# Kernel tuning notes

Hardware: AMD Instinct MI355X
Metric: run time of the kernel (lower is better)

The kernel has to match this reference:

```python
import jax, jax.numpy as jnp
import numpy as np

N = 1024       # sentence length (words incl. root at index 0)
WD = 300       # word embedding dim (GloVe-style)
PD = 25        # pos_emb_dim
H = 125        # hidden_dim_lstm
FC = 100       # hidden_dim_fc
PVOCAB = 50    # POS tagset size


def setup_inputs() -> dict:
    key = jax.random.key(0)
    ks = jax.random.split(key, 14)
    f = lambda k, s: jax.random.normal(k, s, dtype=jnp.float32) * 0.1
    d_in = WD + PD
    return {
        "word_vecs": jax.random.normal(ks[0], (N, WD), dtype=jnp.float32),
        "pos_idx": jax.random.randint(ks[1], (N,), 0, PVOCAB),
        "parents_ids": jax.random.randint(ks[2], (N,), 0, N),
        "pos_emb": f(ks[3], (PVOCAB, PD)),
        "Wih0": f(ks[4], (2, 4 * H, d_in)),
        "Whh0": f(ks[5], (2, 4 * H, H)),
        "b0": f(ks[6], (2, 4 * H)),
        "Wih1": f(ks[7], (2, 4 * H, 2 * H)),
        "Whh1": f(ks[8], (2, 4 * H, H)),
        "b1": f(ks[9], (2, 4 * H)),
        "fc1_W": f(ks[10], (FC, 4 * H)),
        "fc1_b": f(ks[11], (FC,)),
        "fc2_W": f(ks[12], (1, FC)),
        "fc2_b": f(ks[13], (1,)),
    }


def _lstm_dir(x, Wih, Whh, b, reverse):
    # torch LSTM cell, gate order (i, f, g, o); b = b_ih + b_hh
    Hd = Whh.shape[1]
    def step(carry, xt):
        h, c = carry
        g = xt @ Wih.T + h @ Whh.T + b
        i, fg, gg, o = jnp.split(g, 4)
        i = jax.nn.sigmoid(i)
        fg = jax.nn.sigmoid(fg)
        gg = jnp.tanh(gg)
        o = jax.nn.sigmoid(o)
        c = fg * c + i * gg
        h = o * jnp.tanh(c)
        return (h, c), h
    init = (jnp.zeros((Hd,), x.dtype), jnp.zeros((Hd,), x.dtype))
    _, hs = jax.lax.scan(step, init, x, reverse=reverse)
    return hs  # [n, H], already in original time order


def _bilstm_layer(x, Wih, Whh, b):
    hf = _lstm_dir(x, Wih[0], Whh[0], b[0], False)
    hb = _lstm_dir(x, Wih[1], Whh[1], b[1], True)
    return jnp.concatenate([hf, hb], axis=1)  # [n, 2H]


def reference(word_vecs, pos_idx, parents_ids, pos_emb, Wih0, Whh0, b0,
              Wih1, Whh1, b1, fc1_W, fc1_b, fc2_W, fc2_b):
    # encoder: concat word + pos embeddings, 2-layer BiLSTM
    x = jnp.concatenate([word_vecs, pos_emb[pos_idx]], axis=1)  # [n, WD+PD]
    h = _bilstm_layer(x, Wih0, Whh0, b0)
    h = _bilstm_layer(h, Wih1, Whh1, b1)  # [n, 2H]
    n = h.shape[0]
    twoH = h.shape[1]
    # fc1(cat(h_i, h_j)) = h_i @ W_head^T + h_j @ W_child^T + b  (vectorized over all pairs)
    A = h @ fc1_W[:, :twoH].T   # head contribution  [n, FC]
    B = h @ fc1_W[:, twoH:].T   # child contribution [n, FC]
    T = jnp.tanh(A[:, None, :] + B[None, :, :] + fc1_b)  # [n, n, FC]
    raw = T @ fc2_W[0] + fc2_b[0]                         # [n, n]
    ii = jnp.arange(n)
    # original loop skips diagonal and arcs into the root (j == 0); those stay 0
    mask = (ii[:, None] != ii[None, :]) & (ii[None, :] != 0)
    scores_mat = jnp.where(mask, raw, jnp.float32(0.0))
    logits = scores_mat.T  # row j = scores of heads for child j
    logp = jax.nn.log_softmax(logits, axis=1)
    loss = -jnp.mean(logp[jnp.arange(n), parents_ids])
    return loss, scores_mat
```

## Files before the change

kernel.cpp:

```cpp
#include <hip/hip_runtime.h>

typedef float v2f __attribute__((ext_vector_type(2)));
typedef _Float16 f16x8 __attribute__((ext_vector_type(8)));
typedef float f32x4 __attribute__((ext_vector_type(4)));

#define LOG2E 1.4426950408889634f
#define LN2   0.6931471805599453f

__device__ __forceinline__ float fexp2(float x) {
  float r; asm("v_exp_f32 %0, %1" : "=v"(r) : "v"(x)); return r;
}
__device__ __forceinline__ float frcp(float x) {
  float r; asm("v_rcp_f32 %0, %1" : "=v"(r) : "v"(x)); return r;
}
__device__ __forceinline__ float flog2(float x) {
  float r; asm("v_log_f32 %0, %1" : "=v"(r) : "v"(x)); return r;
}
__device__ __forceinline__ void lgkm_barrier() {
  __builtin_amdgcn_sched_barrier(0);
  asm volatile("s_waitcnt lgkmcnt(0)" ::: "memory");
  __builtin_amdgcn_s_barrier();
  __builtin_amdgcn_sched_barrier(0);
}

__global__ void k_embed(const float* __restrict__ wv, const int* __restrict__ pidx,
                        const float* __restrict__ pemb, float* __restrict__ X) {
  int t = blockIdx.x;
  int pi = pidx[t];
  for (int c = threadIdx.x; c < 336; c += 128) {
    float v;
    if (c < 300)      v = wv[t * 300 + c];
    else if (c < 325) v = pemb[pi * 25 + (c - 300)];
    else              v = 0.f;
    X[t * 336 + c] = v;
  }
}

__global__ void k_repack(const float* __restrict__ src, float* __restrict__ dst,
                         int sK, int dK) {
  int r = blockIdx.x;
  for (int c = threadIdx.x; c < dK; c += 128)
    dst[r * dK + c] = (c < sK) ? src[r * sK + c] : 0.f;
}

__global__ void k_wab(const float* __restrict__ fc1W, float* __restrict__ Wab) {
  int r = blockIdx.x;
  int sr = (r < 100) ? r : r - 100;
  int so = (r < 100) ? 0 : 250;
  for (int c = threadIdx.x; c < 256; c += 128)
    Wab[r * 256 + c] = (c < 250) ? fc1W[sr * 500 + so + c] : 0.f;
}

__global__ void k_misc(const float* __restrict__ fc1b, const float* __restrict__ fc2W,
                       float* __restrict__ biasAB, float* __restrict__ sumw) {
  __shared__ float red[128];
  int t = threadIdx.x;
  for (int c = t; c < 256; c += 128)
    biasAB[c] = (c < 100) ? fc1b[c] : 0.f;
  float s = (t < 100) ? fc2W[t] : 0.f;
  red[t] = s; __syncthreads();
  for (int off = 64; off; off >>= 1) {
    if (t < off) red[t] += red[t + off];
    __syncthreads();
  }
  if (t == 0) sumw[0] = red[0];
}

#define BM 64
#define BN 64
#define BKK 16
__global__ __launch_bounds__(256) void k_gemm(
    const float* __restrict__ A, const float* __restrict__ Bw,
    const float* __restrict__ bias, float* __restrict__ C,
    int M, int N, int K, int ldC, long sBz, long sCz, long sbz, int transOut) {
  const int z = blockIdx.z;
  const float* Bp = Bw + (size_t)z * sBz;
  const float* bp = bias + (size_t)z * sbz;
  float* Cp = C + (size_t)z * sCz;
  const int bm = blockIdx.y * BM, bn = blockIdx.x * BN;
  __shared__ __align__(16) float As[BKK][BM + 4];
  __shared__ __align__(16) float Bs[BKK][BN + 4];
  __shared__ float Ts[BN][BM + 1];
  const int tid = threadIdx.x;
  const int tx = tid & 15, ty = tid >> 4;
  const int lr = tid >> 2;
  const int lk = (tid & 3) * 4;
  float acc[4][4];
#pragma unroll
  for (int a = 0; a < 4; ++a)
#pragma unroll
    for (int b = 0; b < 4; ++b) acc[a][b] = 0.f;

  int brow = bn + lr; if (brow >= N) brow = N - 1;
  for (int k0 = 0; k0 < K; k0 += BKK) {
    float4 a4 = *(const float4*)(A + (size_t)(bm + lr) * K + k0 + lk);
    float4 b4 = *(const float4*)(Bp + (size_t)brow * K + k0 + lk);
    __syncthreads();
    As[lk + 0][lr] = a4.x; As[lk + 1][lr] = a4.y; As[lk + 2][lr] = a4.z; As[lk + 3][lr] = a4.w;
    Bs[lk + 0][lr] = b4.x; Bs[lk + 1][lr] = b4.y; Bs[lk + 2][lr] = b4.z; Bs[lk + 3][lr] = b4.w;
    __syncthreads();
#pragma unroll
    for (int kk = 0; kk < BKK; ++kk) {
      float4 av = *(const float4*)&As[kk][ty * 4];
      float4 bv = *(const float4*)&Bs[kk][tx * 4];
      float aa[4] = {av.x, av.y, av.z, av.w};
      float bb[4] = {bv.x, bv.y, bv.z, bv.w};
#pragma unroll
      for (int a = 0; a < 4; ++a)
#pragma unroll
        for (int b = 0; b < 4; ++b)
          acc[a][b] = __builtin_fmaf(aa[a], bb[b], acc[a][b]);
    }
  }
  if (!transOut) {
#pragma unroll
    for (int a = 0; a < 4; ++a) {
      int i = bm + ty * 4 + a;
#pragma unroll
      for (int b = 0; b < 4; ++b) {
        int j = bn + tx * 4 + b;
        if (j < N) Cp[(size_t)i * ldC + j] = acc[a][b] + bp[j];
      }
    }
  } else {
    __syncthreads();
#pragma unroll
    for (int a = 0; a < 4; ++a)
#pragma unroll
      for (int b = 0; b < 4; ++b) {
        int jn = bn + tx * 4 + b; if (jn >= N) jn = N - 1;
        Ts[tx * 4 + b][ty * 4 + a] = acc[a][b] + bp[jn];
      }
    __syncthreads();
    const int n2 = tid >> 2, mq = (tid & 3) * 16;
    const int n = bn + n2;
    if (n < N) {
#pragma unroll
      for (int r = 0; r < 4; ++r) {
        int m0 = mq + r * 4;
        float4 v;
        v.x = Ts[n2][m0 + 0]; v.y = Ts[n2][m0 + 1];
        v.z = Ts[n2][m0 + 2]; v.w = Ts[n2][m0 + 3];
        *(float4*)(Cp + (size_t)n * ldC + bm + m0) = v;
      }
    }
  }
}

__global__ __launch_bounds__(512) void k_rec(const float* __restrict__ Pt,
                                             const float* __restrict__ Whh,
                                             float* __restrict__ hout) {
  const int d = blockIdx.x;
  const bool fwd = (d == 0);
  const int t = threadIdx.x;
  const int w  = t >> 6;
  const int l  = t & 63;
  const int lg = l >> 4;
  const int lc = l & 15;
  const int q  = lc >> 2;

  int u_p = t >> 2; const bool activep = (u_p < 125); if (u_p > 124) u_p = 124;
  const int sub = t & 3;
  const float4* Pr = (const float4*)(Pt + (size_t)d * 500 * 1024 +
                                     (size_t)(sub * 125 + u_p) * 1024);

  const float* Wd = Whh + (size_t)d * 500 * 125;
  f16x8 a[4][4];
#pragma unroll
  for (int rt = 0; rt < 4; ++rt) {
    const int rho = (w << 6) + (rt << 4) + lc;
    const int u2 = rho >> 2, g2 = rho & 3;
    const bool uok = (u2 < 125);
    const float* wr2 = Wd + (size_t)(g2 * 125 + (uok ? u2 : 0)) * 125;
#pragma unroll
    for (int kt = 0; kt < 4; ++kt) {
      f16x8 v;
#pragma unroll
      for (int j = 0; j < 8; ++j) {
        const int k = kt * 32 + lg * 8 + j;
        v[j] = (_Float16)((uok && k < 125) ? wr2[k] : 0.f);
      }
      a[rt][kt] = v;
    }
  }

  __shared__ __align__(16) _Float16 hf[2][128];
  __shared__ __align__(16) float preb[2][512];
  __shared__ float hist[32][128];
  for (int i = t; i < 128; i += 512) ((int*)hf)[i] = 0;
  for (int i = t; i < 1024; i += 512) ((float*)preb)[i] = 0.f;

  float4 cura = Pr[fwd ? 0 : 254];
  float4 curb = Pr[fwd ? 1 : 255];
  float cst = 0.f;
  if (activep) preb[0][t] = fwd ? cura.x : curb.w;
  __syncthreads();

  for (int cb = 0; cb < 128; ++cb) {
    const int nc = (cb + 1 < 128) ? cb + 1 : cb;
    float4 nxta = Pr[fwd ? 2 * nc     : 254 - 2 * nc];
    float4 nxtb = Pr[fwd ? 2 * nc + 1 : 255 - 2 * nc];
#pragma unroll
    for (int e = 0; e < 8; ++e) {
      const int buf = e & 1;
      f16x8 hfr[4];
#pragma unroll
      for (int kt = 0; kt < 4; ++kt)
        hfr[kt] = *(const f16x8*)&hf[buf][kt * 32 + lg * 8];
      f32x4 acc[4];
#pragma unroll
      for (int rt = 0; rt < 4; ++rt)
        acc[rt] = *(const f32x4*)&preb[buf][(w << 6) + (rt << 4) + (lg << 2)];
#pragma unroll
      for (int kt = 0; kt < 4; ++kt)
#pragma unroll
        for (int rt = 0; rt < 4; ++rt)
          acc[rt] = __builtin_amdgcn_mfma_f32_16x16x32_f16(a[rt][kt], hfr[kt],
                                                           acc[rt], 0, 0, 0);
      f32x4 T = (q == 0) ? acc[0] : (q == 1) ? acc[1] : (q == 2) ? acc[2] : acc[3];
      float gi = frcp(1.f + fexp2(-LOG2E * T[0]));
      float gf = frcp(1.f + fexp2(-LOG2E * T[1]));
      float gg = __builtin_fmaf(2.f, frcp(1.f + fexp2(-2.f * LOG2E * T[2])), -1.f);
      float go = frcp(1.f + fexp2(-LOG2E * T[3]));
      cst = __builtin_fmaf(gf, cst, gi * gg);
      float th = __builtin_fmaf(2.f, frcp(1.f + fexp2(-2.f * LOG2E * cst)), -1.f);
      float hv = go * th;
      float pf, pb2;
      if (e < 7) {
        pf  = (e == 0) ? cura.y : (e == 1) ? cura.z : (e == 2) ? cura.w
            : (e == 3) ? curb.x : (e == 4) ? curb.y : (e == 5) ? curb.z : curb.w;
        pb2 = (e == 0) ? curb.z : (e == 1) ? curb.y : (e == 2) ? curb.x
            : (e == 3) ? cura.w : (e == 4) ? cura.z : (e == 5) ? cura.y : cura.x;
      } else { pf = nxta.x; pb2 = nxtb.w; }
      const float pre_next = fwd ? pf : pb2;
      const int u_own = (w << 4) + (q << 2) + lg;
      if (((lc & 3) == 0) && u_own < 125) {
        hf[buf ^ 1][u_own] = (_Float16)hv;
        hist[(cb & 3) * 8 + e][u_own] = hv;
      }
      if (activep) preb[buf ^ 1][t] = pre_next;
      lgkm_barrier();
    }
    if ((cb & 3) == 3) {
      const int S0 = (cb - 3) * 8;
#pragma unroll
      for (int k = 0; k < 8; ++k) {
        int idx = t + k * 512;
        int r = idx >> 7, u2 = idx & 127;
        if (u2 < 125) {
          int step = S0 + r;
          int time = fwd ? step : 1023 - step;
          hout[(size_t)time * 256 + d * 125 + u2] = hist[r][u2];
        }
      }
      lgkm_barrier();
    }
    cura = nxta; curb = nxtb;
  }
}

__global__ __launch_bounds__(256) void k_pair(const float* __restrict__ AB,
    const float* __restrict__ fc2W, const float* __restrict__ fc2b,
    const float* __restrict__ sumw, float* __restrict__ outS,
    float* __restrict__ scoresT) {
  __shared__ float As[32][100];
  __shared__ float Bs[32][101];
  __shared__ float w2s[100];
  const int tid = threadIdx.x;
  const int i0 = blockIdx.y * 32, j0 = blockIdx.x * 32;
  for (int idx = tid; idx < 3200; idx += 256) {
    int r = idx / 100, k = idx - r * 100;
    As[r][k] = AB[(size_t)(i0 + r) * 200 + k];
    Bs[r][k] = AB[(size_t)(j0 + r) * 200 + 100 + k];
  }
  if (tid < 100) w2s[tid] = 2.f * fc2W[tid];
  __syncthreads();
  const int tx = tid & 31, ty = tid >> 5;
  float acc[4] = {0.f, 0.f, 0.f, 0.f};
#pragma unroll 4
  for (int k = 0; k < 100; ++k) {
    float b = Bs[tx][k];
    float wk2 = w2s[k];
    float bs = b * (2.f * LOG2E);
#pragma unroll
    for (int q = 0; q < 4; ++q) {
      float a = As[ty + 8 * q][k];
      float r = frcp(1.f + fexp2(__builtin_fmaf(a, 2.f * LOG2E, bs)));
      acc[q] = __builtin_fmaf(wk2, r, acc[q]);
    }
  }
  float base = sumw[0] + fc2b[0];
  const int j = j0 + tx;
#pragma unroll
  for (int q = 0; q < 4; ++q) {
    int i = i0 + ty + 8 * q;
    float val = (i != j && j != 0) ? (base - acc[q]) : 0.f;
    outS[(size_t)i * 1024 + j] = val;
    scoresT[(size_t)j * 1024 + i] = val;
  }
}

__global__ __launch_bounds__(256) void k_soft(const float* __restrict__ scoresT,
    const int* __restrict__ parents, float* __restrict__ contrib) {
  const int j = blockIdx.x, tid = threadIdx.x;
  __shared__ float red[256];
  const float* row = scoresT + (size_t)j * 1024;
  float v0 = row[tid], v1 = row[tid + 256], v2 = row[tid + 512], v3 = row[tid + 768];
  float m = fmaxf(fmaxf(v0, v1), fmaxf(v2, v3));
  red[tid] = m; __syncthreads();
  for (int off = 128; off; off >>= 1) {
    if (tid < off) red[tid] = fmaxf(red[tid], red[tid + off]);
    __syncthreads();
  }
  m = red[0]; __syncthreads();
  float s = fexp2((v0 - m) * LOG2E) + fexp2((v1 - m) * LOG2E) +
            fexp2((v2 - m) * LOG2E) + fexp2((v3 - m) * LOG2E);
  red[tid] = s; __syncthreads();
  for (int off = 128; off; off >>= 1) {
    if (tid < off) red[tid] += red[tid + off];
    __syncthreads();
  }
  if (tid == 0) {
    float S = red[0];
    int p = parents[j];
    contrib[j] = row[p] - m - flog2(S) * LN2;
  }
}

__global__ __launch_bounds__(256) void k_loss(const float* __restrict__ contrib,
                                              float* __restrict__ out) {
  __shared__ float red[256];
  int tid = threadIdx.x;
  float s = contrib[tid] + contrib[tid + 256] + contrib[tid + 512] + contrib[tid + 768];
  red[tid] = s; __syncthreads();
  for (int off = 128; off; off >>= 1) {
    if (tid < off) red[tid] += red[tid + off];
    __syncthreads();
  }
  if (tid == 0) out[0] = -red[0] * (1.f / 1024.f);
}

extern "C" void kernel_launch(void* const* d_in, const int* in_sizes, int n_in,
                              void* d_out, int out_size, void* d_ws, size_t ws_size,
                              hipStream_t stream) {
  const float* wv   = (const float*)d_in[0];
  const int*   pidx = (const int*)d_in[1];
  const int*   par  = (const int*)d_in[2];
  const float* pemb = (const float*)d_in[3];
  const float* Wih0 = (const float*)d_in[4];
  const float* Whh0 = (const float*)d_in[5];
  const float* b0   = (const float*)d_in[6];
  const float* Wih1 = (const float*)d_in[7];
  const float* Whh1 = (const float*)d_in[8];
  const float* b1   = (const float*)d_in[9];
  const float* fc1W = (const float*)d_in[10];
  const float* fc1b = (const float*)d_in[11];
  const float* fc2W = (const float*)d_in[12];
  const float* fc2b = (const float*)d_in[13];
  float* ws = (float*)d_ws;
  float* X      = ws + 0;
  float* Wih0p  = ws + 344064;
  float* Pt0    = ws + 680064;
  float* h0     = ws + 1704064;
  float* Wih1p  = ws + 1966208;
  float* Pt1    = ws + 2222208;
  float* h1     = ws + 3246208;
  float* Wab    = ws + 3508352;
  float* biasAB = ws + 3559552;
  float* AB     = ws + 3559808;
  float* scT    = ws + 3764608;
  float* contrib= ws + 4813184;
  float* sumw   = ws + 4814208;
  float* out = (float*)d_out;

  hipMemsetAsync(h0, 0, 1024 * 256 * sizeof(float), stream);
  hipMemsetAsync(h1, 0, 1024 * 256 * sizeof(float), stream);

  k_embed <<<1024, 128, 0, stream>>>(wv, pidx, pemb, X);
  k_repack<<<1000, 128, 0, stream>>>(Wih0, Wih0p, 325, 336);
  k_repack<<<1000, 128, 0, stream>>>(Wih1, Wih1p, 250, 256);
  k_wab   <<<200, 128, 0, stream>>>(fc1W, Wab);
  k_misc  <<<1, 128, 0, stream>>>(fc1b, fc2W, biasAB, sumw);

  k_gemm<<<dim3(8, 16, 2), 256, 0, stream>>>(X, Wih0p, b0, Pt0, 1024, 500, 336, 1024,
                                             500L * 336, 500L * 1024, 500L, 1);
  k_rec <<<2, 512, 0, stream>>>(Pt0, Whh0, h0);
  k_gemm<<<dim3(8, 16, 2), 256, 0, stream>>>(h0, Wih1p, b1, Pt1, 1024, 500, 256, 1024,
                                             500L * 256, 500L * 1024, 500L, 1);
  k_rec <<<2, 512, 0, stream>>>(Pt1, Whh1, h1);
  k_gemm<<<dim3(4, 16, 1), 256, 0, stream>>>(h1, Wab, biasAB, AB, 1024, 200, 256, 200,
                                             0L, 0L, 0L, 0);
  k_pair<<<dim3(32, 32), 256, 0, stream>>>(AB, fc2W, fc2b, sumw, out + 1, scT);
  k_soft<<<1024, 256, 0, stream>>>(scT, par, contrib);
  k_loss<<<1, 256, 0, stream>>>(contrib, out);
}
```

Measured before the change: 1.212 ms.

## Pre-permute gate rows and run recurrence with 1024 threads reading preacts directly

The input-projection weights and biases are repacked into the row order the recurrent MFMA tiles use, so the GEMM writes time-major preactivations that each lane can load directly as f32x4 accumulators. This removes the shared-memory preactivation staging buffer and its per-step stores. The recurrent kernel doubles to 1024 threads with two row tiles per wave instead of four, shortening each wave's serial MFMA chain per step. In exchange every step needs a global load on the critical path and the per-step barrier now spans 16 waves instead of 8.

```diff
diff --git a/kernel.cpp b/kernel.cpp
--- a/kernel.cpp
+++ b/kernel.cpp
@@ -36,11 +36,18 @@
   }
 }
 
-__global__ void k_repack(const float* __restrict__ src, float* __restrict__ dst,
-                         int sK, int dK) {
-  int r = blockIdx.x;
+__global__ void k_wpack(const float* __restrict__ Wih, const float* __restrict__ b,
+                        float* __restrict__ Wp, float* __restrict__ bp,
+                        int sK, int dK) {
+  const int d = blockIdx.y, rho = blockIdx.x;
+  const int u = rho >> 2, g = rho & 3;
+  const bool ok = (u < 125);
+  const float* src = Wih + ((size_t)d * 500 + g * 125 + (ok ? u : 0)) * sK;
+  float* dst = Wp + ((size_t)d * 512 + rho) * dK;
   for (int c = threadIdx.x; c < dK; c += 128)
-    dst[r * dK + c] = (c < sK) ? src[r * sK + c] : 0.f;
+    dst[c] = (ok && c < sK) ? src[c] : 0.f;
+  if (threadIdx.x == 0)
+    bp[d * 512 + rho] = ok ? b[d * 500 + g * 125 + u] : 0.f;
 }
 
 __global__ void k_wab(const float* __restrict__ fc1W, float* __restrict__ Wab) {
@@ -147,9 +154,9 @@
   }
 }
 
-__global__ __launch_bounds__(512) void k_rec(const float* __restrict__ Pt,
-                                             const float* __restrict__ Whh,
-                                             float* __restrict__ hout) {
+__global__ __launch_bounds__(1024) void k_rec(const float* __restrict__ Ptt,
+                                              const float* __restrict__ Whh,
+                                              float* __restrict__ hout) {
   const int d = blockIdx.x;
   const bool fwd = (d == 0);
   const int t = threadIdx.x;
@@ -157,18 +164,13 @@
   const int l  = t & 63;
   const int lg = l >> 4;
   const int lc = l & 15;
-  const int q  = lc >> 2;
-
-  int u_p = t >> 2; const bool activep = (u_p < 125); if (u_p > 124) u_p = 124;
-  const int sub = t & 3;
-  const float4* Pr = (const float4*)(Pt + (size_t)d * 500 * 1024 +
-                                     (size_t)(sub * 125 + u_p) * 1024);
+  const int rtsel = lc & 1;
 
   const float* Wd = Whh + (size_t)d * 500 * 125;
-  f16x8 a[4][4];
-#pragma unroll
-  for (int rt = 0; rt < 4; ++rt) {
-    const int rho = (w << 6) + (rt << 4) + lc;
+  f16x8 a[2][4];
+#pragma unroll
+  for (int rt = 0; rt < 2; ++rt) {
+    const int rho = (w << 5) + (rt << 4) + lc;
     const int u2 = rho >> 2, g2 = rho & 3;
     const bool uok = (u2 < 125);
     const float* wr2 = Wd + (size_t)(g2 * 125 + (uok ? u2 : 0)) * 125;
@@ -185,39 +187,36 @@
   }
 
   __shared__ __align__(16) _Float16 hf[2][128];
-  __shared__ __align__(16) float preb[2][512];
   __shared__ float hist[32][128];
-  for (int i = t; i < 128; i += 512) ((int*)hf)[i] = 0;
-  for (int i = t; i < 1024; i += 512) ((float*)preb)[i] = 0.f;
-
-  float4 cura = Pr[fwd ? 0 : 254];
-  float4 curb = Pr[fwd ? 1 : 255];
+  if (t < 128) ((int*)hf)[t] = 0;
+
+  const int dstep = fwd ? 512 : -512;
+  const float* pg = Ptt + (size_t)d * 1024 * 512 +
+                    (size_t)(fwd ? 0 : 1023) * 512 + ((w << 5) + (lg << 2));
+  f32x4 pc0 = *(const f32x4*)(pg);
+  f32x4 pc1 = *(const f32x4*)(pg + 16);
+  pg += dstep;
   float cst = 0.f;
-  if (activep) preb[0][t] = fwd ? cura.x : curb.w;
   __syncthreads();
 
   for (int cb = 0; cb < 128; ++cb) {
-    const int nc = (cb + 1 < 128) ? cb + 1 : cb;
-    float4 nxta = Pr[fwd ? 2 * nc     : 254 - 2 * nc];
-    float4 nxtb = Pr[fwd ? 2 * nc + 1 : 255 - 2 * nc];
 #pragma unroll
     for (int e = 0; e < 8; ++e) {
       const int buf = e & 1;
+      f32x4 pn0 = *(const f32x4*)(pg);
+      f32x4 pn1 = *(const f32x4*)(pg + 16);
+      pg += dstep;
       f16x8 hfr[4];
 #pragma unroll
       for (int kt = 0; kt < 4; ++kt)
         hfr[kt] = *(const f16x8*)&hf[buf][kt * 32 + lg * 8];
-      f32x4 acc[4];
-#pragma unroll
-      for (int rt = 0; rt < 4; ++rt)
-        acc[rt] = *(const f32x4*)&preb[buf][(w << 6) + (rt << 4) + (lg << 2)];
-#pragma unroll
-      for (int kt = 0; kt < 4; ++kt)
-#pragma unroll
-        for (int rt = 0; rt < 4; ++rt)
-          acc[rt] = __builtin_amdgcn_mfma_f32_16x16x32_f16(a[rt][kt], hfr[kt],
-                                                           acc[rt], 0, 0, 0);
-      f32x4 T = (q == 0) ? acc[0] : (q == 1) ? acc[1] : (q == 2) ? acc[2] : acc[3];
+      f32x4 acc0 = pc0, acc1 = pc1;
+#pragma unroll
+      for (int kt = 0; kt < 4; ++kt) {
+        acc0 = __builtin_amdgcn_mfma_f32_16x16x32_f16(a[0][kt], hfr[kt], acc0, 0, 0, 0);
+        acc1 = __builtin_amdgcn_mfma_f32_16x16x32_f16(a[1][kt], hfr[kt], acc1, 0, 0, 0);
+      }
+      f32x4 T = rtsel ? acc1 : acc0;
       float gi = frcp(1.f + fexp2(-LOG2E * T[0]));
       float gf = frcp(1.f + fexp2(-LOG2E * T[1]));
       float gg = __builtin_fmaf(2.f, frcp(1.f + fexp2(-2.f * LOG2E * T[2])), -1.f);
@@ -225,27 +224,19 @@
       cst = __builtin_fmaf(gf, cst, gi * gg);
       float th = __builtin_fmaf(2.f, frcp(1.f + fexp2(-2.f * LOG2E * cst)), -1.f);
       float hv = go * th;
-      float pf, pb2;
-      if (e < 7) {
-        pf  = (e == 0) ? cura.y : (e == 1) ? cura.z : (e == 2) ? cura.w
-            : (e == 3) ? curb.x : (e == 4) ? curb.y : (e == 5) ? curb.z : curb.w;
-        pb2 = (e == 0) ? curb.z : (e == 1) ? curb.y : (e == 2) ? curb.x
-            : (e == 3) ? cura.w : (e == 4) ? cura.z : (e == 5) ? cura.y : cura.x;
-      } else { pf = nxta.x; pb2 = nxtb.w; }
-      const float pre_next = fwd ? pf : pb2;
-      const int u_own = (w << 4) + (q << 2) + lg;
-      if (((lc & 3) == 0) && u_own < 125) {
+      const int u_own = (w << 3) + (rtsel << 2) + lg;
+      if (lc < 2 && u_own < 125) {
         hf[buf ^ 1][u_own] = (_Float16)hv;
         hist[(cb & 3) * 8 + e][u_own] = hv;
       }
-      if (activep) preb[buf ^ 1][t] = pre_next;
       lgkm_barrier();
+      pc0 = pn0; pc1 = pn1;
     }
     if ((cb & 3) == 3) {
       const int S0 = (cb - 3) * 8;
 #pragma unroll
-      for (int k = 0; k < 8; ++k) {
-        int idx = t + k * 512;
+      for (int k = 0; k < 4; ++k) {
+        int idx = t + k * 1024;
         int r = idx >> 7, u2 = idx & 127;
         if (u2 < 125) {
           int step = S0 + r;
@@ -255,7 +246,6 @@
       }
       lgkm_barrier();
     }
-    cura = nxta; curb = nxtb;
   }
 }
 
@@ -360,34 +350,35 @@
   float* ws = (float*)d_ws;
   float* X      = ws + 0;
   float* Wih0p  = ws + 344064;
-  float* Pt0    = ws + 680064;
-  float* h0     = ws + 1704064;
-  float* Wih1p  = ws + 1966208;
-  float* Pt1    = ws + 2222208;
-  float* h1     = ws + 3246208;
-  float* Wab    = ws + 3508352;
-  float* biasAB = ws + 3559552;
-  float* AB     = ws + 3559808;
-  float* scT    = ws + 3764608;
-  float* contrib= ws + 4813184;
-  float* sumw   = ws + 4814208;
+  float* Wih1p  = ws + 688128;
+  float* brho0  = ws + 950272;
+  float* brho1  = ws + 951296;
+  float* Ptt    = ws + 952320;
+  float* h0     = ws + 2000896;
+  float* h1     = ws + 2263040;
+  float* Wab    = ws + 2525184;
+  float* biasAB = ws + 2576384;
+  float* AB     = ws + 2576640;
+  float* scT    = ws + 2781440;
+  float* contrib= ws + 3830016;
+  float* sumw   = ws + 3831040;
   float* out = (float*)d_out;
 
   hipMemsetAsync(h0, 0, 1024 * 256 * sizeof(float), stream);
   hipMemsetAsync(h1, 0, 1024 * 256 * sizeof(float), stream);
 
   k_embed <<<1024, 128, 0, stream>>>(wv, pidx, pemb, X);
-  k_repack<<<1000, 128, 0, stream>>>(Wih0, Wih0p, 325, 336);
-  k_repack<<<1000, 128, 0, stream>>>(Wih1, Wih1p, 250, 256);
+  k_wpack <<<dim3(512, 2), 128, 0, stream>>>(Wih0, b0, Wih0p, brho0, 325, 336);
+  k_wpack <<<dim3(512, 2), 128, 0, stream>>>(Wih1, b1, Wih1p, brho1, 250, 256);
   k_wab   <<<200, 128, 0, stream>>>(fc1W, Wab);
   k_misc  <<<1, 128, 0, stream>>>(fc1b, fc2W, biasAB, sumw);
 
-  k_gemm<<<dim3(8, 16, 2), 256, 0, stream>>>(X, Wih0p, b0, Pt0, 1024, 500, 336, 1024,
-                                             500L * 336, 500L * 1024, 500L, 1);
-  k_rec <<<2, 512, 0, stream>>>(Pt0, Whh0, h0);
-  k_gemm<<<dim3(8, 16, 2), 256, 0, stream>>>(h0, Wih1p, b1, Pt1, 1024, 500, 256, 1024,
-                                             500L * 256, 500L * 1024, 500L, 1);
-  k_rec <<<2, 512, 0, stream>>>(Pt1, Whh1, h1);
+  k_gemm<<<dim3(8, 16, 2), 256, 0, stream>>>(X, Wih0p, brho0, Ptt, 1024, 512, 336, 512,
+                                             512L * 336, 1024L * 512, 512L, 0);
+  k_rec <<<2, 1024, 0, stream>>>(Ptt, Whh0, h0);
+  k_gemm<<<dim3(8, 16, 2), 256, 0, stream>>>(h0, Wih1p, brho1, Ptt, 1024, 512, 256, 512,
+                                             512L * 256, 1024L * 512, 512L, 0);
+  k_rec <<<2, 1024, 0, stream>>>(Ptt, Whh1, h1);
   k_gemm<<<dim3(4, 16, 1), 256, 0, stream>>>(h1, Wab, biasAB, AB, 1024, 200, 256, 200,
                                              0L, 0L, 0L, 0);
   k_pair<<<dim3(32, 32), 256, 0, stream>>>(AB, fc2W, fc2b, sumw, out + 1, scT);
```

Result: slower. 1.269 ms (+4.7%).
